# Kernel optimization log

Hardware: AMD Instinct MI355X
Metric: run time of the kernel (lower is better)

The kernel has to match this reference:

```python
import jax, jax.numpy as jnp
import numpy as np

NX, NY, NZ = 512, 512, 1
C = 64          # num_bev_features
B = 4           # batch size
P = 120000      # total non-empty pillars across the batch


def setup_inputs() -> dict:
    key = jax.random.key(0)
    k_feat, k_perm = jax.random.split(key)
    pillar_features = jax.random.normal(k_feat, (P, C), dtype=jnp.float32)
    # Unique (batch, cell) slots so the indexed-assignment scatter is well-defined.
    flat = jax.random.permutation(k_perm, B * NZ * NX * NY)[:P]
    b = flat // (NZ * NX * NY)
    pos = flat % (NZ * NX * NY)          # = y * nx + x (nz == 1)
    y = pos // NX
    x = pos % NX
    z = jnp.zeros_like(b)                # nz == 1 -> z coord is always 0
    voxel_coords = jnp.stack([b, z, y, x], axis=1).astype(jnp.int32)  # [P, 4]
    return {"pillar_features": pillar_features,
            "voxel_coords": voxel_coords,
            "batch_size": B}


def reference(pillar_features, voxel_coords, batch_size):
    # Fused global scatter: flat index = batch * (nz*nx*ny) + (c1 + c2*nx + c3),
    # exactly replicating indices = coords[:,1] + coords[:,2]*nx + coords[:,3].
    cells = NZ * NX * NY
    idx = (voxel_coords[:, 1] + voxel_coords[:, 2] * NX + voxel_coords[:, 3]).astype(jnp.int32)
    flat = voxel_coords[:, 0].astype(jnp.int32) * cells + idx     # [P]
    grid = jnp.zeros((batch_size * cells, C), dtype=pillar_features.dtype)
    grid = grid.at[flat].set(pillar_features)                     # [B*cells, C]
    # (B, cells, C) -> (B, C, cells) -> (B, C*nz, ny, nx), matching the torch view.
    out = grid.reshape(batch_size, cells, C).transpose(0, 2, 1)
    return out.reshape(batch_size, C * NZ, NY, NX)
```

## Files before the change

kernel.cpp:

```cpp
#include <hip/hip_runtime.h>


#define G_NX 512
#define G_NY 512
#define G_C 64
#define G_B 4
#define G_CELLS (G_NX * G_NY)

typedef float fv4 __attribute__((ext_vector_type(4)));

__global__ __launch_bounds__(256) void ppscatter_map_kernel(
    const int* __restrict__ coords, int* __restrict__ map, int P) {
  int p = blockIdx.x * blockDim.x + threadIdx.x;
  if (p >= P) return;
  int4 cr = ((const int4*)coords)[p];
  map[cr.x * G_CELLS + (cr.y + cr.z * G_NX + cr.w)] = p;
}

__global__ __launch_bounds__(256) void ppscatter_gather_kernel(
    const float* __restrict__ feat, const int* __restrict__ map,
    float* __restrict__ out) {
  const int b = blockIdx.y;
  const int cell0 = blockIdx.x * 1024 + threadIdx.x * 4;

  int4 p4 = *(const int4*)(map + b * G_CELLS + cell0);
  float* orow = out + (size_t)b * (G_C * G_CELLS) + cell0;
  const fv4* f4 = (const fv4*)feat;

  const long q0 = (long)p4.x * 16, q1 = (long)p4.y * 16;
  const long q2 = (long)p4.z * 16, q3 = (long)p4.w * 16;
  const fv4 z4 = {0.f, 0.f, 0.f, 0.f};

#pragma unroll
  for (int cg = 0; cg < 16; ++cg) {
    fv4 r0 = (p4.x >= 0) ? f4[q0 + cg] : z4;
    fv4 r1 = (p4.y >= 0) ? f4[q1 + cg] : z4;
    fv4 r2 = (p4.z >= 0) ? f4[q2 + cg] : z4;
    fv4 r3 = (p4.w >= 0) ? f4[q3 + cg] : z4;

    fv4 s0 = {r0.x, r1.x, r2.x, r3.x};
    fv4 s1 = {r0.y, r1.y, r2.y, r3.y};
    fv4 s2 = {r0.z, r1.z, r2.z, r3.z};
    fv4 s3 = {r0.w, r1.w, r2.w, r3.w};

    __builtin_nontemporal_store(s0, (fv4*)(orow + (size_t)(4 * cg + 0) * G_CELLS));
    __builtin_nontemporal_store(s1, (fv4*)(orow + (size_t)(4 * cg + 1) * G_CELLS));
    __builtin_nontemporal_store(s2, (fv4*)(orow + (size_t)(4 * cg + 2) * G_CELLS));
    __builtin_nontemporal_store(s3, (fv4*)(orow + (size_t)(4 * cg + 3) * G_CELLS));
  }
}

extern "C" void kernel_launch(void* const* d_in, const int* in_sizes, int n_in,
                              void* d_out, int out_size, void* d_ws, size_t ws_size,
                              hipStream_t stream) {
  const float* feat = (const float*)d_in[0];
  const int* coords = (const int*)d_in[1];
  float* out = (float*)d_out;

  const int P = in_sizes[0] / G_C;
  int* map = (int*)d_ws;

  (void)hipMemsetAsync(map, 0xFF, (size_t)G_B * G_CELLS * sizeof(int), stream);
  ppscatter_map_kernel<<<(P + 255) / 256, 256, 0, stream>>>(coords, map, P);
  ppscatter_gather_kernel<<<dim3(G_CELLS / 1024, G_B), 256, 0, stream>>>(
      feat, map, out);
}
```

Baseline: 296.4 us.

## Split gather kernel channels across grid z and batch feature loads upfront

```diff
diff --git a/kernel.cpp b/kernel.cpp
--- a/kernel.cpp
+++ b/kernel.cpp
@@ -21,32 +21,40 @@
     const float* __restrict__ feat, const int* __restrict__ map,
     float* __restrict__ out) {
   const int b = blockIdx.y;
+  const int cg0 = blockIdx.z * 4;
   const int cell0 = blockIdx.x * 1024 + threadIdx.x * 4;
 
   int4 p4 = *(const int4*)(map + b * G_CELLS + cell0);
-  float* orow = out + (size_t)b * (G_C * G_CELLS) + cell0;
+  float* orow = out + (size_t)b * (G_C * G_CELLS) +
+                (size_t)(4 * cg0) * G_CELLS + cell0;
   const fv4* f4 = (const fv4*)feat;
 
-  const long q0 = (long)p4.x * 16, q1 = (long)p4.y * 16;
-  const long q2 = (long)p4.z * 16, q3 = (long)p4.w * 16;
+  const long q0 = (long)p4.x * 16 + cg0;
+  const long q1 = (long)p4.y * 16 + cg0;
+  const long q2 = (long)p4.z * 16 + cg0;
+  const long q3 = (long)p4.w * 16 + cg0;
   const fv4 z4 = {0.f, 0.f, 0.f, 0.f};
 
+  fv4 r0[4], r1[4], r2[4], r3[4];
 #pragma unroll
-  for (int cg = 0; cg < 16; ++cg) {
-    fv4 r0 = (p4.x >= 0) ? f4[q0 + cg] : z4;
-    fv4 r1 = (p4.y >= 0) ? f4[q1 + cg] : z4;
-    fv4 r2 = (p4.z >= 0) ? f4[q2 + cg] : z4;
-    fv4 r3 = (p4.w >= 0) ? f4[q3 + cg] : z4;
+  for (int k = 0; k < 4; ++k) {
+    r0[k] = (p4.x >= 0) ? f4[q0 + k] : z4;
+    r1[k] = (p4.y >= 0) ? f4[q1 + k] : z4;
+    r2[k] = (p4.z >= 0) ? f4[q2 + k] : z4;
+    r3[k] = (p4.w >= 0) ? f4[q3 + k] : z4;
+  }
 
-    fv4 s0 = {r0.x, r1.x, r2.x, r3.x};
-    fv4 s1 = {r0.y, r1.y, r2.y, r3.y};
-    fv4 s2 = {r0.z, r1.z, r2.z, r3.z};
-    fv4 s3 = {r0.w, r1.w, r2.w, r3.w};
-
-    __builtin_nontemporal_store(s0, (fv4*)(orow + (size_t)(4 * cg + 0) * G_CELLS));
-    __builtin_nontemporal_store(s1, (fv4*)(orow + (size_t)(4 * cg + 1) * G_CELLS));
-    __builtin_nontemporal_store(s2, (fv4*)(orow + (size_t)(4 * cg + 2) * G_CELLS));
-    __builtin_nontemporal_store(s3, (fv4*)(orow + (size_t)(4 * cg + 3) * G_CELLS));
+#pragma unroll
+  for (int k = 0; k < 4; ++k) {
+    fv4 s0 = {r0[k].x, r1[k].x, r2[k].x, r3[k].x};
+    fv4 s1 = {r0[k].y, r1[k].y, r2[k].y, r3[k].y};
+    fv4 s2 = {r0[k].z, r1[k].z, r2[k].z, r3[k].z};
+    fv4 s3 = {r0[k].w, r1[k].w, r2[k].w, r3[k].w};
+    float* oc = orow + (size_t)(4 * k) * G_CELLS;
+    __builtin_nontemporal_store(s0, (fv4*)(oc + 0 * (size_t)G_CELLS));
+    __builtin_nontemporal_store(s1, (fv4*)(oc + 1 * (size_t)G_CELLS));
+    __builtin_nontemporal_store(s2, (fv4*)(oc + 2 * (size_t)G_CELLS));
+    __builtin_nontemporal_store(s3, (fv4*)(oc + 3 * (size_t)G_CELLS));
   }
 }
 
@@ -62,6 +70,6 @@
 
   (void)hipMemsetAsync(map, 0xFF, (size_t)G_B * G_CELLS * sizeof(int), stream);
   ppscatter_map_kernel<<<(P + 255) / 256, 256, 0, stream>>>(coords, map, P);
-  ppscatter_gather_kernel<<<dim3(G_CELLS / 1024, G_B), 256, 0, stream>>>(
+  ppscatter_gather_kernel<<<dim3(G_CELLS / 1024, G_B, 4), 256, 0, stream>>>(
       feat, map, out);
 }
```

After: 295.8 us. No clear change (-0.2%).
